# Performance work log

Hardware: AMD Instinct MI355X
Metric: run time of the kernel (lower is better)

The kernel has to match this reference:

```python
import jax, jax.numpy as jnp
import numpy as np

B, LD = 256, 64
NO, LO = 10240, 32
NM, LM = 81920, 16
EO, EM = 81920, 327680
E, HID, H, Dh, V = 128, 256, 8, 16, 10000


def masked_mean(tokens, table):
    # tokens: [N, L] int; pad id = 0
    emb = table[tokens]                            # [N, L, E]
    mask = (tokens != 0)
    s = jnp.sum(emb * mask[..., None].astype(emb.dtype), axis=1)
    lens = jnp.maximum(jnp.sum(mask, axis=1), 1).astype(emb.dtype)
    return s / lens[:, None]


def segment_softmax(scores, seg, num_segments):
    # scores: [E, ...]; softmax over entries sharing seg id (PyG softmax)
    m = jax.ops.segment_max(scores, seg, num_segments=num_segments)
    e = jnp.exp(scores - m[seg])
    s = jax.ops.segment_sum(e, seg, num_segments=num_segments)
    return e / (s[seg] + 1e-16)


def gcn_conv(x, W, b, src, dst, n):
    # PyG GCNConv: normalize=True, add_self_loops=True
    xw = x @ W
    loops = jnp.arange(n, dtype=src.dtype)
    s2 = jnp.concatenate([src, loops])
    d2 = jnp.concatenate([dst, loops])
    deg = jax.ops.segment_sum(jnp.ones_like(d2, dtype=x.dtype), d2, num_segments=n)
    dinv = deg ** -0.5  # deg >= 1 due to self loops
    norm = dinv[s2] * dinv[d2]
    out = jax.ops.segment_sum(xw[s2] * norm[:, None], d2, num_segments=n)
    return out + b


def transformer_conv(x, Wq, bq, Wk, bk, Wv, bv, Wskip, bskip, src, dst, n):
    q = (x @ Wq + bq).reshape(n, H, Dh)
    k = (x @ Wk + bk).reshape(n, H, Dh)
    v = (x @ Wv + bv).reshape(n, H, Dh)
    score = jnp.sum(q[dst] * k[src], axis=-1) / jnp.sqrt(jnp.asarray(Dh, x.dtype))  # [E, H]
    alpha = segment_softmax(score, dst, n)
    agg = jax.ops.segment_sum(alpha[:, :, None] * v[src], dst, num_segments=n)  # [n, H, Dh]
    return agg.reshape(n, H * Dh) + x @ Wskip + bskip


def global_attention(x, Wg, bg, seg, num_segments):
    gate = x @ Wg + bg                              # [N, 1]
    a = segment_softmax(gate, seg, num_segments)
    return jax.ops.segment_sum(a * x, seg, num_segments=num_segments)


def setup_inputs():
    key = jax.random.key(0)
    ks = jax.random.split(key, 20)
    sc = lambda k, shape: jax.random.normal(k, shape, dtype=jnp.float32) * 0.05
    inp = {
        "desc_tokens": jax.random.randint(ks[0], (B, LD), 0, V, dtype=jnp.int32),
        "x_tokens": jax.random.randint(ks[1], (NO, LO), 0, V, dtype=jnp.int32),
        "mini_tokens": jax.random.randint(ks[2], (NM, LM), 0, V, dtype=jnp.int32),
        "src": jax.random.randint(ks[3], (EO,), 0, NO, dtype=jnp.int32),
        "dst": jax.random.randint(ks[4], (EO,), 0, NO, dtype=jnp.int32),
        "mini_src": jax.random.randint(ks[5], (EM,), 0, NM, dtype=jnp.int32),
        "mini_dst": jax.random.randint(ks[6], (EM,), 0, NM, dtype=jnp.int32),
        "mini_batch": (jnp.arange(NM, dtype=jnp.int32) // (NM // NO)),
        "node_batch": (jnp.arange(NO, dtype=jnp.int32) // (NO // B)),
        "desc_table": sc(ks[7], (V, E)),
        "code_table": sc(ks[8], (V, E)),
        "code_table2": sc(ks[9], (V, E)),
        "Wq": sc(ks[10], (E, H * Dh)), "bq": jnp.zeros((H * Dh,), jnp.float32),
        "Wk": sc(ks[11], (E, H * Dh)), "bk": jnp.zeros((H * Dh,), jnp.float32),
        "Wv": sc(ks[12], (E, H * Dh)), "bv": jnp.zeros((H * Dh,), jnp.float32),
        "Wskip": sc(ks[13], (E, H * Dh)), "bskip": jnp.zeros((H * Dh,), jnp.float32),
        "W2": sc(ks[14], (E, HID)), "b2": jnp.zeros((HID,), jnp.float32),
        "W3": sc(ks[15], (HID, E)), "b3": jnp.zeros((E,), jnp.float32),
        "Wg": sc(ks[16], (E, 1)), "bg": jnp.zeros((1,), jnp.float32),
    }
    return inp


def reference(desc_tokens, x_tokens, mini_tokens, src, dst, mini_src, mini_dst,
              mini_batch, node_batch, desc_table, code_table, code_table2,
              Wq, bq, Wk, bk, Wv, bv, Wskip, bskip, W2, b2, W3, b3, Wg, bg):
    # encode_desc: embedding + masked mean pool -> [B, E]
    h_n = masked_mean(desc_tokens, desc_table)
    # encode_code_graph
    stmt_emb = masked_mean(x_tokens, code_table2)          # [NO, E]
    mini_emb = masked_mean(mini_tokens, code_table)        # [NM, E]
    mini_hidden = transformer_conv(mini_emb, Wq, bq, Wk, bk, Wv, bv,
                                   Wskip, bskip, mini_src, mini_dst, NM)
    mini_fn = global_attention(mini_hidden, Wg, bg, mini_batch, NO)  # [NO, E]
    mini_fn = (mini_fn + stmt_emb) * 0.5
    h = jax.nn.relu(gcn_conv(mini_fn, W2, b2, src, dst, NO))
    final_stmt = gcn_conv(h, W3, b3, src, dst, NO)
    fn_repr = global_attention(final_stmt, Wg, bg, node_batch, B)    # [B, E]
    # cosine similarity (torch eps=1e-8 clamps each norm)
    na = jnp.maximum(jnp.linalg.norm(fn_repr, axis=-1), 1e-8)
    nb = jnp.maximum(jnp.linalg.norm(h_n, axis=-1), 1e-8)
    return jnp.sum(fn_repr * h_n, axis=-1) / (na * nb)
```

## Files before the change

kernel.cpp:

```cpp
#include <hip/hip_runtime.h>
#include <hip/hip_bf16.h>
#include <math.h>

#define BB   256
#define LDE  64
#define NO   10240
#define LO   32
#define NM   81920
#define LM   16
#define EO   81920
#define EM   327680
#define ED   128
#define HIDD 256
#define NH   8
#define DH   16
#define VV   10000

static inline int nblk(long long n, int b) { return (int)((n + b - 1) / b); }

typedef __attribute__((ext_vector_type(8))) short short8;
typedef __attribute__((ext_vector_type(4))) float f32x4;

static __device__ __forceinline__ unsigned short bf16_rne(float f) {
  unsigned u = __float_as_uint(f);
  return (unsigned short)((u + 0x7fffu + ((u >> 16) & 1u)) >> 16);
}
static __device__ __forceinline__ float bf16_to_f(unsigned short h) {
  return __uint_as_float(((unsigned)h) << 16);
}
static __device__ __forceinline__ float4 b4f(ushort4 h) {
  return make_float4(bf16_to_f(h.x), bf16_to_f(h.y), bf16_to_f(h.z), bf16_to_f(h.w));
}
static __device__ __forceinline__ ushort4 f4b(float4 v) {
  return make_ushort4(bf16_rne(v.x), bf16_rne(v.y), bf16_rne(v.z), bf16_rne(v.w));
}

static __device__ __forceinline__ void gl_lds16(const void* g, void* l) {
  __builtin_amdgcn_global_load_lds(
      (const __attribute__((address_space(1))) unsigned int*)g,
      (__attribute__((address_space(3))) unsigned int*)l, 16, 0, 0);
}

struct ConvArgs {
  const float *Wq, *Wk, *Wv, *Ws, *W2, *W3;
  const float *bq, *bk, *bv, *bs;
  short8* frag;
  float* bias512;
  const float* t1; unsigned short* o1;
  const float* t2; unsigned short* o2;
  int* hist;
};
#define TBLK (2 * VV * ED / 4 / 256)
#define ZBLK ((NM + NO) / 256)
__global__ void __launch_bounds__(256)
conv_all_k(ConvArgs A) {
  int b = blockIdx.x;
  if (b < 32) {
    int g = b * 256 + threadIdx.x;
    int lane = g & 63, f = g >> 6;
    int jl = f & 7, kb = (f >> 3) & 3, ch = f >> 5;
    int cf = ch * 8 + jl;
    int c = cf * 16 + (lane & 15);
    int k0 = kb * 32 + ((lane >> 4) << 3);
    const float* wp; int cm;
    if (c < 128)      { wp = A.Wq; cm = c; }
    else if (c < 384) { int u = c - 128, t = u & 7;
                        wp = (t < 4) ? A.Wk : A.Wv; cm = (u >> 3) * 4 + (t & 3); }
    else              { wp = A.Ws; cm = c - 384; }
    short8 h;
    #pragma unroll
    for (int j = 0; j < 8; ++j)
      h[j] = (short)bf16_rne(wp[(size_t)(k0 + j) * 128 + cm]);
    A.frag[g] = h;
  } else if (b < 64) {
    int g = (b - 32) * 256 + threadIdx.x;
    const float* wp; int M, dstbase, gg;
    if (g < 4096) { wp = A.W2; M = 256; dstbase = 8192;  gg = g; }
    else          { wp = A.W3; M = 128; dstbase = 12288; gg = g - 4096; }
    int lane = gg & 63, fid = gg >> 6;
    int nt = fid % (M / 16), kb = fid / (M / 16);
    int n = nt * 16 + (lane & 15);
    int k0 = kb * 32 + ((lane >> 4) << 3);
    short8 h;
    #pragma unroll
    for (int j = 0; j < 8; ++j)
      h[j] = (short)bf16_rne(wp[(size_t)(k0 + j) * M + n]);
    A.frag[dstbase + gg] = h;
  } else if (b < 64 + TBLK) {
    int q = (b - 64) * 256 + threadIdx.x;
    const int NT = VV * ED / 4;
    if (q < NT) {
      float4 v = *(const float4*)(A.t1 + (size_t)q * 4);
      *(ushort4*)(A.o1 + (size_t)q * 4) = f4b(v);
    } else if (q < 2 * NT) {
      int q2 = q - NT;
      float4 v = *(const float4*)(A.t2 + (size_t)q2 * 4);
      *(ushort4*)(A.o2 + (size_t)q2 * 4) = f4b(v);
    }
  } else if (b < 64 + TBLK + ZBLK) {
    int i = (b - 64 - TBLK) * 256 + threadIdx.x;
    if (i < NM + NO) A.hist[i] = 0;
  } else {
    for (int c = threadIdx.x; c < 512; c += 256) {
      float v;
      if (c < 128)      v = A.bq[c];
      else if (c < 384) { int u = c - 128, t = u & 7;
                          v = (t < 4) ? A.bk[(u >> 3) * 4 + t] : A.bv[(u >> 3) * 4 + (t & 3)]; }
      else              v = A.bs[c - 384];
      A.bias512[c] = v;
    }
  }
}

template<int L>
static __device__ __forceinline__ void embed_body_f(const int* __restrict__ tokens,
                                                    const float* __restrict__ table,
                                                    float* __restrict__ out, int blk) {
  const int r = threadIdx.x >> 5, lane = threadIdx.x & 31;
  const int n0 = blk * 8;
  __shared__ int toks[8][L];
  for (int i = threadIdx.x; i < 8 * L; i += 256)
    toks[i / L][i % L] = tokens[(size_t)n0 * L + i];
  __syncthreads();
  float4 acc = make_float4(0.f, 0.f, 0.f, 0.f);
  int cnt = 0;
  #pragma unroll
  for (int l = 0; l < L; ++l) {
    int t = toks[r][l];
    float4 v = *(const float4*)(table + (size_t)t * ED + lane * 4);
    float msk = (t != 0) ? 1.f : 0.f;
    cnt += (t != 0);
    acc.x = fmaf(msk, v.x, acc.x); acc.y = fmaf(msk, v.y, acc.y);
    acc.z = fmaf(msk, v.z, acc.z); acc.w = fmaf(msk, v.w, acc.w);
  }
  float inv = 1.f / (float)(cnt > 0 ? cnt : 1);
  acc.x *= inv; acc.y *= inv; acc.z *= inv; acc.w *= inv;
  *(float4*)(out + (size_t)(n0 + r) * ED + lane * 4) = acc;
}

template<int L>
static __device__ __forceinline__ void embed_body16(const int* __restrict__ tokens,
                                                    const unsigned short* __restrict__ table,
                                                    unsigned short* __restrict__ out, int blk) {
  const int r = threadIdx.x >> 4, lane = threadIdx.x & 15;
  const int n0 = blk * 16;
  __shared__ int toks[16][L];
  for (int i = threadIdx.x; i < 16 * L; i += 256)
    toks[i / L][i % L] = tokens[(size_t)n0 * L + i];
  __syncthreads();
  float acc[8] = {};
  int cnt = 0;
  #pragma unroll
  for (int l = 0; l < L; ++l) {
    int t = toks[r][l];
    short8 v = *(const short8*)(table + (size_t)t * ED + lane * 8);
    float msk = (t != 0) ? 1.f : 0.f;
    cnt += (t != 0);
    #pragma unroll
    for (int j = 0; j < 8; ++j)
      acc[j] = fmaf(msk, bf16_to_f((unsigned short)v[j]), acc[j]);
  }
  float inv = 1.f / (float)(cnt > 0 ? cnt : 1);
  short8 o;
  #pragma unroll
  for (int j = 0; j < 8; ++j) o[j] = (short)bf16_rne(acc[j] * inv);
  *(short8*)(out + (size_t)(n0 + r) * ED + lane * 8) = o;
}

#define HBLK ((EM + EO) / 256)
#define MBLK (NM / 16)
#define XBLK (NO / 16)
__global__ void __launch_bounds__(256)
embed_all_k(const int* __restrict__ desc_tokens, const float* __restrict__ desc_table,
            float* __restrict__ h_n,
            const int* __restrict__ x_tokens, const unsigned short* __restrict__ ctab2,
            unsigned short* __restrict__ stmt,
            const int* __restrict__ mini_tokens, const unsigned short* __restrict__ ctab,
            unsigned short* __restrict__ miniE,
            const int* __restrict__ mini_dst, const int* __restrict__ dst,
            int* __restrict__ histm, int* __restrict__ histo) {
  int b = blockIdx.x;
  if (b < MBLK) embed_body16<LM>(mini_tokens, ctab, miniE, b);
  else if (b < MBLK + XBLK) embed_body16<LO>(x_tokens, ctab2, stmt, b - MBLK);
  else if (b < MBLK + XBLK + BB / 8)
    embed_body_f<LDE>(desc_tokens, desc_table, h_n, b - MBLK - XBLK);
  else {
    int e = (b - MBLK - XBLK - BB / 8) * 256 + threadIdx.x;
    if (e < EM) atomicAdd(&histm[mini_dst[e]], 1);
    else        atomicAdd(&histo[dst[e - EM]], 1);
  }
}

__global__ void __launch_bounds__(256)
scan_final2_k(const int* __restrict__ hist, const int* __restrict__ part,
              int* __restrict__ offsm, int* __restrict__ curm,
              int* __restrict__ offso, int* __restrict__ curo,
              float* __restrict__ dinv) {
  __shared__ int sd[256], red[256];
  const int b = blockIdx.x, t = threadIdx.x;
  const int i = b * 256 + t;
  const int v = hist[i];
  sd[t] = v; __syncthreads();
  for (int off = 1; off < 256; off <<= 1) {
    int a = (t >= off) ? sd[t - off] : 0;
    __syncthreads(); sd[t] += a; __syncthreads();
  }
  const int excl = sd[t] - v;
  const int segBase = (b < NM / 256) ? 0 : NM / 256;
  const int myIdx = b - segBase;
  int s = 0;
  for (int k = t; k < myIdx; k += 256) s += part[segBase + k];
  red[t] = s; __syncthreads();
  for (int o = 128; o > 0; o >>= 1) { if (t < o) red[t] += red[t + o]; __syncthreads(); }
  const int off = red[0] + excl;
  if (i < NM) {
    offsm[i] = off; curm[i] = off;
    if (i == NM - 1) offsm[NM] = off + v;
  } else {
    int i2 = i - NM;
    offso[i2] = off; curo[i2] = off;
    if (i2 == NO - 1) offso[NO] = off + v;
    dinv[i2] = 1.f / sqrtf(1.f + (float)v);
  }
}
__global__ void scatter2_k(const int* __restrict__ sm, const int* __restrict__ dm,
                           int* __restrict__ cm, int* __restrict__ km,
                           const int* __restrict__ so, const int* __restrict__ dd,
                           int* __restrict__ co, int* __restrict__ ko) {
  int e = blockIdx.x * 256 + threadIdx.x;
  if (e < EM) {
    int pos = atomicAdd(&cm[dm[e]], 1);
    km[pos] = sm[e];
  } else {
    int e2 = e - EM;
    if (e2 < EO) {
      int pos = atomicAdd(&co[dd[e2]], 1);
      ko[pos] = so[e2];
    }
  }
}

#define QKVSB (NM / 128)
#define CSUMB ((NM + NO) / 256)
__global__ void __launch_bounds__(512)
qkvs_merged_k(const unsigned short* __restrict__ Ab, const short8* __restrict__ Wf,
              const float* __restrict__ bias512, unsigned short* __restrict__ out,
              const int* __restrict__ hist, int* __restrict__ part) {
  __shared__ short8 wlds[2048];
  const int tid = threadIdx.x;
  if (blockIdx.x >= QKVSB) {
    int* sd = (int*)wlds;
    const int cb = blockIdx.x - QKVSB;
    const int i = cb * 256 + (tid & 255);
    if (tid < 256) sd[tid] = (i < NM + NO) ? hist[i] : 0;
    __syncthreads();
    for (int s = 128; s > 0; s >>= 1) {
      if (tid < s) sd[tid] += sd[tid + s];
      __syncthreads();
    }
    if (tid == 0) part[cb] = sd[0];
    return;
  }
  const int id = blockIdx.x;
  const int blk = (id & 7) * 80 + (id >> 3);
  const int n0 = blk * 128;
  const int w = tid >> 6, lane = tid & 63;
  const int r = lane & 15, qd = lane >> 4;
  const int node = n0 + w * 16 + r;
  char* myl = (char*)wlds + w * 4096;

  short8 a[4];
  #pragma unroll
  for (int kb = 0; kb < 4; ++kb)
    a[kb] = *(const short8*)(Ab + (size_t)node * ED + kb * 32 + qd * 8);

  for (int ch = 0; ch < 4; ++ch) {
    {
      const char* gs = (const char*)Wf + (size_t)ch * 32768
                     + (size_t)(w * 4) * 1024 + (size_t)lane * 16;
      char* ls = (char*)wlds + (w * 4) * 1024;
      #pragma unroll
      for (int t = 0; t < 4; ++t)
        gl_lds16(gs + t * 1024, ls + t * 1024);
    }
    __syncthreads();

    f32x4 acc[8];
    #pragma unroll
    for (int jl = 0; jl < 8; ++jl) acc[jl] = (f32x4){0.f, 0.f, 0.f, 0.f};
    #pragma unroll
    for (int kb = 0; kb < 4; ++kb)
      #pragma unroll
      for (int jl = 0; jl < 8; ++jl) {
        short8 wf = *(const short8*)((const char*)wlds
                      + ((size_t)((kb << 3) | jl) * 64 + lane) * 16);
        acc[jl] = __builtin_amdgcn_mfma_f32_16x16x32_bf16(wf, a[kb], acc[jl], 0, 0, 0);
      }
    __syncthreads();

    #pragma unroll
    for (int jl = 0; jl < 8; ++jl) {
      const int cf = ch * 8 + jl;
      const float4 bv = *(const float4*)(bias512 + cf * 16 + qd * 4);
      ushort4 o;
      o.x = bf16_rne(acc[jl][0] + bv.x);
      o.y = bf16_rne(acc[jl][1] + bv.y);
      o.z = bf16_rne(acc[jl][2] + bv.z);
      o.w = bf16_rne(acc[jl][3] + bv.w);
      *(ushort4*)(myl + r * 256 + ((jl * 32) ^ ((r & 7) << 5)) + qd * 8) = o;
    }
    #pragma unroll
    for (int t = 0; t < 4; ++t) {
      const int rr = t * 4 + qd;
      short8 v = *(const short8*)(myl + rr * 256 + (((lane & 15) * 16) ^ ((rr & 7) << 5)));
      *(short8*)(out + (size_t)(n0 + w * 16 + rr) * 512 + ch * 128 + (lane & 15) * 8) = v;
    }
    __syncthreads();
  }
}

template<bool RELU>
__global__ void __launch_bounds__(512)
mgemm_b_k(const unsigned short* __restrict__ Ab, const short8* __restrict__ Bh,
          const float* __restrict__ bias, unsigned short* __restrict__ C,
          int K, int M) {
  const int bn0 = blockIdx.x * 128;
  const int n0 = blockIdx.y * 128;
  const int tid = threadIdx.x;
  const int w = tid >> 6, lane = tid & 63;
  const int wm = (w & 3) * 2, wn = (w >> 2) * 4;
  const int r = lane & 15, qd = lane >> 4;
  const int NTm = M / 16;
  f32x4 acc[2][4];
  #pragma unroll
  for (int i = 0; i < 2; ++i)
    #pragma unroll
    for (int j = 0; j < 4; ++j) acc[i][j] = (f32x4){0.f, 0.f, 0.f, 0.f};
  const int kbn = K / 32;
  for (int kb = 0; kb < kbn; ++kb) {
    short8 bh[4];
    #pragma unroll
    for (int j = 0; j < 4; ++j)
      bh[j] = Bh[((size_t)kb * NTm + (bn0 >> 4) + wn + j) * 64 + lane];
    short8 a[2];
    #pragma unroll
    for (int i = 0; i < 2; ++i)
      a[i] = *(const short8*)(Ab + (size_t)(n0 + (wm + i) * 16 + r) * K + kb * 32 + qd * 8);
    #pragma unroll
    for (int i = 0; i < 2; ++i)
      #pragma unroll
      for (int j = 0; j < 4; ++j)
        acc[i][j] = __builtin_amdgcn_mfma_f32_16x16x32_bf16(bh[j], a[i], acc[i][j], 0, 0, 0);
  }
  #pragma unroll
  for (int i = 0; i < 2; ++i)
    #pragma unroll
    for (int j = 0; j < 4; ++j) {
      const int node = n0 + (wm + i) * 16 + r;
      const int colb = bn0 + (wn + j) * 16 + qd * 4;
      float4 bv = bias ? *(const float4*)(bias + colb) : make_float4(0.f, 0.f, 0.f, 0.f);
      float v0 = acc[i][j][0] + bv.x;
      float v1 = acc[i][j][1] + bv.y;
      float v2 = acc[i][j][2] + bv.z;
      float v3 = acc[i][j][3] + bv.w;
      if (RELU) {
        v0 = fmaxf(v0, 0.f); v1 = fmaxf(v1, 0.f);
        v2 = fmaxf(v2, 0.f); v3 = fmaxf(v3, 0.f);
      }
      ushort4 o = make_ushort4(bf16_rne(v0), bf16_rne(v1), bf16_rne(v2), bf16_rne(v3));
      *(ushort4*)(C + (size_t)node * M + colb) = o;
    }
}

__global__ void __launch_bounds__(256)
attn_comb_k(const unsigned short* __restrict__ buf,
            const int* __restrict__ offs, const int* __restrict__ csr,
            const float* __restrict__ Wg, const float* __restrict__ bg,
            const unsigned short* __restrict__ stmt, unsigned short* __restrict__ out) {
  const int g = threadIdx.x >> 5, lane = threadIdx.x & 31;
  const int n = blockIdx.x * 8 + g;
  float4 q = b4f(*(const ushort4*)(buf + (size_t)n * 512 + lane * 4));
  float4 sk = b4f(*(const ushort4*)(buf + (size_t)n * 512 + 384 + lane * 4));
  float4 wg = *(const float4*)(Wg + lane * 4);
  int lo = offs[n], hi = offs[n + 1];
  float4 O = make_float4(0.f, 0.f, 0.f, 0.f);
  float m = -INFINITY, l = 0.f;
  for (int base = lo; base < hi; base += 4) {
    int rem = hi - base;
    int sidx[4];
    #pragma unroll
    for (int i = 0; i < 4; ++i) sidx[i] = (i < rem) ? csr[base + i] : 0;
    short8 kvr[4];
    #pragma unroll
    for (int i = 0; i < 4; ++i)
      kvr[i] = *(const short8*)(buf + (size_t)sidx[i] * 512 + 128 + lane * 8);
    float sc[4]; float4 vt[4];
    #pragma unroll
    for (int i = 0; i < 4; ++i) {
      float4 kt = make_float4(bf16_to_f((unsigned short)kvr[i][0]),
                              bf16_to_f((unsigned short)kvr[i][1]),
                              bf16_to_f((unsigned short)kvr[i][2]),
                              bf16_to_f((unsigned short)kvr[i][3]));
      vt[i] = make_float4(bf16_to_f((unsigned short)kvr[i][4]),
                          bf16_to_f((unsigned short)kvr[i][5]),
                          bf16_to_f((unsigned short)kvr[i][6]),
                          bf16_to_f((unsigned short)kvr[i][7]));
      float p = q.x * kt.x + q.y * kt.y + q.z * kt.z + q.w * kt.w;
      p += __shfl_xor(p, 1, 64);
      p += __shfl_xor(p, 2, 64);
      sc[i] = (i < rem) ? p * 0.25f : -INFINITY;
    }
    float mt = fmaxf(fmaxf(sc[0], sc[1]), fmaxf(sc[2], sc[3]));
    float mn = fmaxf(m, mt);
    float scale = __expf(m - mn);
    float pe[4];
    #pragma unroll
    for (int i = 0; i < 4; ++i) pe[i] = __expf(sc[i] - mn);
    l = l * scale + ((pe[0] + pe[1]) + (pe[2] + pe[3]));
    O.x = fmaf(pe[3], vt[3].x, fmaf(pe[2], vt[2].x, fmaf(pe[1], vt[1].x, fmaf(pe[0], vt[0].x, O.x * scale))));
    O.y = fmaf(pe[3], vt[3].y, fmaf(pe[2], vt[2].y, fmaf(pe[1], vt[1].y, fmaf(pe[0], vt[0].y, O.y * scale))));
    O.z = fmaf(pe[3], vt[3].z, fmaf(pe[2], vt[2].z, fmaf(pe[1], vt[1].z, fmaf(pe[0], vt[0].z, O.z * scale))));
    O.w = fmaf(pe[3], vt[3].w, fmaf(pe[2], vt[2].w, fmaf(pe[1], vt[1].w, fmaf(pe[0], vt[0].w, O.w * scale))));
    m = mn;
  }
  float inv = 1.f / (l + 1e-16f);
  float4 ov = make_float4(O.x * inv + sk.x, O.y * inv + sk.y,
                          O.z * inv + sk.z, O.w * inv + sk.w);
  float ps = ov.x * wg.x + ov.y * wg.y + ov.z * wg.z + ov.w * wg.w;
  #pragma unroll
  for (int o = 1; o <= 16; o <<= 1) ps += __shfl_xor(ps, o, 64);
  __shared__ float outs[8][32][4];
  __shared__ float gates[8];
  *(float4*)&outs[g][lane][0] = ov;
  if (lane == 0) gates[g] = ps + bg[0];
  __syncthreads();
  if (threadIdx.x < 32) {
    float gm = -INFINITY;
    #pragma unroll
    for (int j = 0; j < 8; ++j) gm = fmaxf(gm, gates[j]);
    float e[8], s = 0.f;
    #pragma unroll
    for (int j = 0; j < 8; ++j) { e[j] = __expf(gates[j] - gm); s += e[j]; }
    float ia = 1.f / (s + 1e-16f);
    float4 acc = make_float4(0.f, 0.f, 0.f, 0.f);
    #pragma unroll
    for (int j = 0; j < 8; ++j) {
      float a = e[j] * ia;
      float4 v = *(const float4*)&outs[j][threadIdx.x][0];
      acc.x = fmaf(a, v.x, acc.x); acc.y = fmaf(a, v.y, acc.y);
      acc.z = fmaf(a, v.z, acc.z); acc.w = fmaf(a, v.w, acc.w);
    }
    float4 o4 = b4f(*(const ushort4*)(stmt + (size_t)blockIdx.x * ED + threadIdx.x * 4));
    acc.x = (acc.x + o4.x) * 0.5f; acc.y = (acc.y + o4.y) * 0.5f;
    acc.z = (acc.z + o4.z) * 0.5f; acc.w = (acc.w + o4.w) * 0.5f;
    *(ushort4*)(out + (size_t)blockIdx.x * ED + threadIdx.x * 4) = f4b(acc);
  }
}

__global__ void __launch_bounds__(256)
gcn_gather_b_k(const unsigned short* __restrict__ x, const float* __restrict__ dinv,
               const int* __restrict__ offs, const int* __restrict__ csr,
               const float* __restrict__ bias, unsigned short* __restrict__ out,
               const float* __restrict__ Wg, const float* __restrict__ bg,
               float* __restrict__ gateOut) {
  const int wv = threadIdx.x >> 6, lane = threadIdx.x & 63;
  const int half = lane >> 5, cl = lane & 31;
  const int n = blockIdx.x * 4 + wv;
  float di = dinv[n];
  float4 acc = make_float4(0.f, 0.f, 0.f, 0.f);
  if (half == 0) {
    float4 xs = b4f(*(const ushort4*)(x + (size_t)n * ED + cl * 4));
    float w0 = di * di;
    acc = make_float4(w0 * xs.x, w0 * xs.y, w0 * xs.z, w0 * xs.w);
  }
  int lo = offs[n], hi = offs[n + 1];
  for (int base = lo; base < hi; base += 8) {
    int sidx[4]; bool ok[4];
    #pragma unroll
    for (int i = 0; i < 4; ++i) {
      int e = base + 2 * i + half;
      ok[i] = e < hi;
      sidx[i] = ok[i] ? csr[e] : 0;
    }
    float dw[4];
    #pragma unroll
    for (int i = 0; i < 4; ++i) dw[i] = ok[i] ? di * dinv[sidx[i]] : 0.f;
    ushort4 vr[4];
    #pragma unroll
    for (int i = 0; i < 4; ++i)
      vr[i] = *(const ushort4*)(x + (size_t)sidx[i] * ED + cl * 4);
    #pragma unroll
    for (int i = 0; i < 4; ++i) {
      float4 v = b4f(vr[i]);
      acc.x = fmaf(dw[i], v.x, acc.x); acc.y = fmaf(dw[i], v.y, acc.y);
      acc.z = fmaf(dw[i], v.z, acc.z); acc.w = fmaf(dw[i], v.w, acc.w);
    }
  }
  acc.x += __shfl_xor(acc.x, 32, 64); acc.y += __shfl_xor(acc.y, 32, 64);
  acc.z += __shfl_xor(acc.z, 32, 64); acc.w += __shfl_xor(acc.w, 32, 64);
  if (bias) {
    float4 b4 = *(const float4*)(bias + cl * 4);
    acc.x += b4.x; acc.y += b4.y; acc.z += b4.z; acc.w += b4.w;
  }
  if (half == 0)
    *(ushort4*)(out + (size_t)n * ED + cl * 4) = f4b(acc);
  if (gateOut) {
    float4 wg = *(const float4*)(Wg + cl * 4);
    float ps = acc.x * wg.x + acc.y * wg.y + acc.z * wg.z + acc.w * wg.w;
    #pragma unroll
    for (int o = 1; o <= 16; o <<= 1) ps += __shfl_xor(ps, o, 64);
    if (lane == 0) gateOut[n] = ps + bg[0];
  }
}

static __device__ __forceinline__ int lower_bound_d(const int* a, int n, int key) {
  int lo = 0, hi = n;
  while (lo < hi) { int mid = (lo + hi) >> 1; if (a[mid] < key) lo = mid + 1; else hi = mid; }
  return lo;
}
__global__ void __launch_bounds__(128)
gattn_cos_k(const unsigned short* __restrict__ x, const float* __restrict__ gate,
            const int* __restrict__ seg, int Ntot,
            const float* __restrict__ hn, float* __restrict__ outp) {
  const int g = threadIdx.x >> 5, lane = threadIdx.x & 31;
  const int n = blockIdx.x * 4 + g;
  __shared__ int sh[4][2];
  if (lane == 0) {
    sh[g][0] = lower_bound_d(seg, Ntot, n);
    sh[g][1] = lower_bound_d(seg, Ntot, n + 1);
  }
  __syncthreads();
  int lo = sh[g][0], hi = sh[g][1];
  float m = -INFINITY;
  for (int j = lo; j < hi; ++j) m = fmaxf(m, gate[j]);
  float ssum = 0.f;
  for (int j = lo; j < hi; ++j) ssum += __expf(gate[j] - m);
  float inv = 1.f / (ssum + 1e-16f);
  float4 acc = make_float4(0.f, 0.f, 0.f, 0.f);
  for (int j = lo; j < hi; ++j) {
    float a = __expf(gate[j] - m) * inv;
    float4 v = b4f(*(const ushort4*)(x + (size_t)j * ED + lane * 4));
    acc.x = fmaf(a, v.x, acc.x); acc.y = fmaf(a, v.y, acc.y);
    acc.z = fmaf(a, v.z, acc.z); acc.w = fmaf(a, v.w, acc.w);
  }
  float4 hv = *(const float4*)(hn + (size_t)n * ED + lane * 4);
  float dot = acc.x * hv.x + acc.y * hv.y + acc.z * hv.z + acc.w * hv.w;
  float na  = acc.x * acc.x + acc.y * acc.y + acc.z * acc.z + acc.w * acc.w;
  float nb  = hv.x * hv.x + hv.y * hv.y + hv.z * hv.z + hv.w * hv.w;
  #pragma unroll
  for (int o = 1; o <= 16; o <<= 1) {
    dot += __shfl_xor(dot, o, 64);
    na  += __shfl_xor(na,  o, 64);
    nb  += __shfl_xor(nb,  o, 64);
  }
  if (lane == 0)
    outp[n] = dot / (fmaxf(sqrtf(na), 1e-8f) * fmaxf(sqrtf(nb), 1e-8f));
}

constexpr size_t OFF_HN    = 0;
constexpr size_t OFF_STMT  = OFF_HN    + (size_t)BB * ED;
constexpr size_t OFF_A     = OFF_STMT  + (size_t)NO * ED;
constexpr size_t OFF_CT    = OFF_A     + (size_t)NM * ED;
constexpr size_t OFF_QKVS  = OFF_CT    + (size_t)VV * ED;
constexpr size_t T0        = OFF_QKVS  + (size_t)NM * 256;
constexpr size_t OFF_GATE  = T0;
constexpr size_t OFF_GATE2 = OFF_GATE  + (size_t)NM;
constexpr size_t OFF_DINV  = OFF_GATE2 + (size_t)NO;
constexpr size_t OFF_HISTM = OFF_DINV  + (size_t)NO;
constexpr size_t OFF_HISTO = OFF_HISTM + (size_t)NM;
constexpr size_t OFF_OFFSM = OFF_HISTO + (size_t)NO;
constexpr size_t OFF_CURM  = OFF_OFFSM + (size_t)NM + 1;
constexpr size_t OFF_CSRM  = OFF_CURM  + (size_t)NM;
constexpr size_t OFF_OFFSO = OFF_CSRM  + (size_t)EM;
constexpr size_t OFF_CURO  = OFF_OFFSO + (size_t)NO + 1;
constexpr size_t OFF_CSRO  = OFF_CURO  + (size_t)NO;
constexpr size_t OFF_PART  = OFF_CSRO  + (size_t)EO;
constexpr size_t OFF_B512  = OFF_PART  + 512;
constexpr size_t OFF_WFHI  = OFF_B512  + 512;
constexpr size_t OFF_MFN   = OFF_A;
constexpr size_t OFF_AGG   = OFF_MFN   + (size_t)NO * ED;
constexpr size_t OFF_H     = OFF_AGG   + (size_t)NO * ED;
constexpr size_t OFF_T     = OFF_H     + (size_t)NO * HIDD;
constexpr size_t OFF_FIN   = OFF_T     + (size_t)NO * ED;

extern "C" void kernel_launch(void* const* d_in, const int* in_sizes, int n_in,
                              void* d_out, int out_size, void* d_ws, size_t ws_size,
                              hipStream_t stream) {
  const int* desc_tokens = (const int*)d_in[0];
  const int* x_tokens    = (const int*)d_in[1];
  const int* mini_tokens = (const int*)d_in[2];
  const int* src         = (const int*)d_in[3];
  const int* dst         = (const int*)d_in[4];
  const int* mini_src    = (const int*)d_in[5];
  const int* mini_dst    = (const int*)d_in[6];
  const int* mini_batch  = (const int*)d_in[7];
  const int* node_batch  = (const int*)d_in[8];
  const float* desc_table  = (const float*)d_in[9];
  const float* code_table  = (const float*)d_in[10];
  const float* code_table2 = (const float*)d_in[11];
  const float* Wq = (const float*)d_in[12]; const float* bq = (const float*)d_in[13];
  const float* Wk = (const float*)d_in[14]; const float* bk = (const float*)d_in[15];
  const float* Wv = (const float*)d_in[16]; const float* bv = (const float*)d_in[17];
  const float* Wskip = (const float*)d_in[18]; const float* bskip = (const float*)d_in[19];
  const float* W2 = (const float*)d_in[20]; const float* b2 = (const float*)d_in[21];
  const float* W3 = (const float*)d_in[22]; const float* b3 = (const float*)d_in[23];
  const float* Wg = (const float*)d_in[24]; const float* bg = (const float*)d_in[25];
  (void)mini_batch;

  float* ws = (float*)d_ws;
  float* h_n   = ws + OFF_HN;
  unsigned short* stmt_b  = (unsigned short*)(ws + OFF_STMT);
  unsigned short* miniE_b = (unsigned short*)(ws + OFF_A);
  unsigned short* ctab_b  = (unsigned short*)(ws + OFF_CT);
  unsigned short* ctab2_b = ctab_b + (size_t)VV * ED;
  unsigned short* qkvs_b  = (unsigned short*)(ws + OFF_QKVS);
  float* gate2 = ws + OFF_GATE2;
  float* dinv  = ws + OFF_DINV;
  int* histm = (int*)(ws + OFF_HISTM);
  int* histo = (int*)(ws + OFF_HISTO);
  int* offsm = (int*)(ws + OFF_OFFSM);
  int* curm  = (int*)(ws + OFF_CURM);
  int* csrm  = (int*)(ws + OFF_CSRM);
  int* offso = (int*)(ws + OFF_OFFSO);
  int* curo  = (int*)(ws + OFF_CURO);
  int* csro  = (int*)(ws + OFF_CSRO);
  int* part  = (int*)(ws + OFF_PART);
  float* bias512 = ws + OFF_B512;
  short8* wfrag = (short8*)(ws + OFF_WFHI);
  unsigned short* mini_fn_b = (unsigned short*)(ws + OFF_MFN);
  unsigned short* aggb_b    = (unsigned short*)(ws + OFF_AGG);
  unsigned short* hbuf_b    = (unsigned short*)(ws + OFF_H);
  unsigned short* tbuf_b    = (unsigned short*)(ws + OFF_T);
  unsigned short* finalS_b  = (unsigned short*)(ws + OFF_FIN);
  float* outp    = (float*)d_out;

  ConvArgs ca;
  ca.Wq = Wq; ca.Wk = Wk; ca.Wv = Wv; ca.Ws = Wskip; ca.W2 = W2; ca.W3 = W3;
  ca.bq = bq; ca.bk = bk; ca.bv = bv; ca.bs = bskip;
  ca.frag = wfrag; ca.bias512 = bias512;
  ca.t1 = code_table;  ca.o1 = ctab_b;
  ca.t2 = code_table2; ca.o2 = ctab2_b;
  ca.hist = histm;
  conv_all_k<<<64 + TBLK + ZBLK + 1, 256, 0, stream>>>(ca);

  embed_all_k<<<MBLK + XBLK + BB / 8 + HBLK, 256, 0, stream>>>(
      desc_tokens, desc_table, h_n, x_tokens, ctab2_b, stmt_b,
      mini_tokens, ctab_b, miniE_b, mini_dst, dst, histm, histo);

  qkvs_merged_k<<<QKVSB + CSUMB, 512, 0, stream>>>(miniE_b, wfrag, bias512, qkvs_b,
                                                   histm, part);

  scan_final2_k<<<(NM + NO) / 256, 256, 0, stream>>>(histm, part, offsm, curm,
                                                     offso, curo, dinv);
  scatter2_k<<<nblk(EM + EO, 256), 256, 0, stream>>>(mini_src, mini_dst, curm, csrm,
                                                     src, dst, curo, csro);

  attn_comb_k<<<NO, 256, 0, stream>>>(qkvs_b, offsm, csrm, Wg, bg, stmt_b, mini_fn_b);

  gcn_gather_b_k<<<NO / 4, 256, 0, stream>>>(mini_fn_b, dinv, offso, csro, nullptr,
                                             aggb_b, nullptr, nullptr, nullptr);
  { dim3 g(HIDD / 128, NO / 128);
    mgemm_b_k<true><<<g, 512, 0, stream>>>(aggb_b, wfrag + 8192, b2, hbuf_b, ED, HIDD); }

  { dim3 g(1, NO / 128);
    mgemm_b_k<false><<<g, 512, 0, stream>>>(hbuf_b, wfrag + 12288, nullptr, tbuf_b, HIDD, ED); }
  gcn_gather_b_k<<<NO / 4, 256, 0, stream>>>(tbuf_b, dinv, offso, csro, b3, finalS_b,
                                             Wg, bg, gate2);

  gattn_cos_k<<<BB / 4, 128, 0, stream>>>(finalS_b, gate2, node_batch, NO, h_n, outp);
}
```

Measured before the change: 311.8 us.

## Fuse first GCN gather with both dense layers into one kernel

Replaces the first GCN gather plus the two MFMA GEMM launches with one kernel. Each 512-thread block aggregates 128 nodes into LDS, runs the W2 GEMM with bias and ReLU into LDS, then runs the W3 GEMM and writes the result. This removes two launches and the global round trips for the aggregated and hidden buffers. In exchange the grid shrinks to only 80 blocks, which leaves most of the GPU idle during the latency-bound gather phase.

```diff
diff --git a/kernel.cpp b/kernel.cpp
--- a/kernel.cpp
+++ b/kernel.cpp
@@ -319,59 +319,6 @@
   }
 }
 
-template<bool RELU>
-__global__ void __launch_bounds__(512)
-mgemm_b_k(const unsigned short* __restrict__ Ab, const short8* __restrict__ Bh,
-          const float* __restrict__ bias, unsigned short* __restrict__ C,
-          int K, int M) {
-  const int bn0 = blockIdx.x * 128;
-  const int n0 = blockIdx.y * 128;
-  const int tid = threadIdx.x;
-  const int w = tid >> 6, lane = tid & 63;
-  const int wm = (w & 3) * 2, wn = (w >> 2) * 4;
-  const int r = lane & 15, qd = lane >> 4;
-  const int NTm = M / 16;
-  f32x4 acc[2][4];
-  #pragma unroll
-  for (int i = 0; i < 2; ++i)
-    #pragma unroll
-    for (int j = 0; j < 4; ++j) acc[i][j] = (f32x4){0.f, 0.f, 0.f, 0.f};
-  const int kbn = K / 32;
-  for (int kb = 0; kb < kbn; ++kb) {
-    short8 bh[4];
-    #pragma unroll
-    for (int j = 0; j < 4; ++j)
-      bh[j] = Bh[((size_t)kb * NTm + (bn0 >> 4) + wn + j) * 64 + lane];
-    short8 a[2];
-    #pragma unroll
-    for (int i = 0; i < 2; ++i)
-      a[i] = *(const short8*)(Ab + (size_t)(n0 + (wm + i) * 16 + r) * K + kb * 32 + qd * 8);
-    #pragma unroll
-    for (int i = 0; i < 2; ++i)
-      #pragma unroll
-      for (int j = 0; j < 4; ++j)
-        acc[i][j] = __builtin_amdgcn_mfma_f32_16x16x32_bf16(bh[j], a[i], acc[i][j], 0, 0, 0);
-  }
-  #pragma unroll
-  for (int i = 0; i < 2; ++i)
-    #pragma unroll
-    for (int j = 0; j < 4; ++j) {
-      const int node = n0 + (wm + i) * 16 + r;
-      const int colb = bn0 + (wn + j) * 16 + qd * 4;
-      float4 bv = bias ? *(const float4*)(bias + colb) : make_float4(0.f, 0.f, 0.f, 0.f);
-      float v0 = acc[i][j][0] + bv.x;
-      float v1 = acc[i][j][1] + bv.y;
-      float v2 = acc[i][j][2] + bv.z;
-      float v3 = acc[i][j][3] + bv.w;
-      if (RELU) {
-        v0 = fmaxf(v0, 0.f); v1 = fmaxf(v1, 0.f);
-        v2 = fmaxf(v2, 0.f); v3 = fmaxf(v3, 0.f);
-      }
-      ushort4 o = make_ushort4(bf16_rne(v0), bf16_rne(v1), bf16_rne(v2), bf16_rne(v3));
-      *(ushort4*)(C + (size_t)node * M + colb) = o;
-    }
-}
-
 __global__ void __launch_bounds__(256)
 attn_comb_k(const unsigned short* __restrict__ buf,
             const int* __restrict__ offs, const int* __restrict__ csr,
@@ -454,6 +401,101 @@
     acc.x = (acc.x + o4.x) * 0.5f; acc.y = (acc.y + o4.y) * 0.5f;
     acc.z = (acc.z + o4.z) * 0.5f; acc.w = (acc.w + o4.w) * 0.5f;
     *(ushort4*)(out + (size_t)blockIdx.x * ED + threadIdx.x * 4) = f4b(acc);
+  }
+}
+
+__global__ void __launch_bounds__(512)
+mlp_fused_k(const unsigned short* __restrict__ x,
+            const float* __restrict__ dinv,
+            const int* __restrict__ offs, const int* __restrict__ csr,
+            const short8* __restrict__ W2f, const float* __restrict__ b2,
+            const short8* __restrict__ W3f,
+            unsigned short* __restrict__ tout) {
+  __shared__ char buf[128 * 512];
+  const int tid = threadIdx.x;
+  const int w = tid >> 6, lane = tid & 63;
+  const int half = lane >> 5, cl = lane & 31;
+  const int n0 = blockIdx.x * 128;
+
+  for (int i = 0; i < 16; ++i) {
+    const int rl = w * 16 + i;
+    const int n = n0 + rl;
+    float di = dinv[n];
+    float4 acc = make_float4(0.f, 0.f, 0.f, 0.f);
+    if (half == 0) {
+      float4 xs = b4f(*(const ushort4*)(x + (size_t)n * ED + cl * 4));
+      float w0 = di * di;
+      acc = make_float4(w0 * xs.x, w0 * xs.y, w0 * xs.z, w0 * xs.w);
+    }
+    int lo = offs[n], hi = offs[n + 1];
+    for (int base = lo; base < hi; base += 8) {
+      int sidx[4]; bool ok[4];
+      #pragma unroll
+      for (int t = 0; t < 4; ++t) {
+        int e = base + 2 * t + half;
+        ok[t] = e < hi;
+        sidx[t] = ok[t] ? csr[e] : 0;
+      }
+      float dw[4];
+      #pragma unroll
+      for (int t = 0; t < 4; ++t) dw[t] = ok[t] ? di * dinv[sidx[t]] : 0.f;
+      ushort4 vr[4];
+      #pragma unroll
+      for (int t = 0; t < 4; ++t)
+        vr[t] = *(const ushort4*)(x + (size_t)sidx[t] * ED + cl * 4);
+      #pragma unroll
+      for (int t = 0; t < 4; ++t) {
+        float4 v = b4f(vr[t]);
+        acc.x = fmaf(dw[t], v.x, acc.x); acc.y = fmaf(dw[t], v.y, acc.y);
+        acc.z = fmaf(dw[t], v.z, acc.z); acc.w = fmaf(dw[t], v.w, acc.w);
+      }
+    }
+    acc.x += __shfl_xor(acc.x, 32, 64); acc.y += __shfl_xor(acc.y, 32, 64);
+    acc.z += __shfl_xor(acc.z, 32, 64); acc.w += __shfl_xor(acc.w, 32, 64);
+    if (half == 0)
+      *(ushort4*)(buf + rl * 256 + ((cl * 8) ^ ((rl & 7) << 4))) = f4b(acc);
+  }
+  __syncthreads();
+
+  const int r = lane & 15, qd = lane >> 4;
+  const int row = w * 16 + r;
+  short8 a1[4];
+  #pragma unroll
+  for (int kb = 0; kb < 4; ++kb)
+    a1[kb] = *(const short8*)(buf + row * 256 + ((kb * 64 + qd * 16) ^ ((row & 7) << 4)));
+  __syncthreads();
+
+  #pragma unroll 4
+  for (int cf = 0; cf < 16; ++cf) {
+    f32x4 acc = (f32x4){0.f, 0.f, 0.f, 0.f};
+    #pragma unroll
+    for (int kb = 0; kb < 4; ++kb)
+      acc = __builtin_amdgcn_mfma_f32_16x16x32_bf16(
+          W2f[((size_t)(kb * 16 + cf)) * 64 + lane], a1[kb], acc, 0, 0, 0);
+    const float4 bv = *(const float4*)(b2 + cf * 16 + qd * 4);
+    ushort4 o;
+    o.x = bf16_rne(fmaxf(acc[0] + bv.x, 0.f));
+    o.y = bf16_rne(fmaxf(acc[1] + bv.y, 0.f));
+    o.z = bf16_rne(fmaxf(acc[2] + bv.z, 0.f));
+    o.w = bf16_rne(fmaxf(acc[3] + bv.w, 0.f));
+    *(ushort4*)(buf + row * 512 + ((cf * 32 + qd * 8) ^ ((row & 7) << 4))) = o;
+  }
+  __syncthreads();
+
+  short8 a2[8];
+  #pragma unroll
+  for (int kb = 0; kb < 8; ++kb)
+    a2[kb] = *(const short8*)(buf + row * 512 + ((kb * 64 + qd * 16) ^ ((row & 7) << 4)));
+  #pragma unroll
+  for (int cf = 0; cf < 8; ++cf) {
+    f32x4 acc = (f32x4){0.f, 0.f, 0.f, 0.f};
+    #pragma unroll
+    for (int kb = 0; kb < 8; ++kb)
+      acc = __builtin_amdgcn_mfma_f32_16x16x32_bf16(
+          W3f[((size_t)(kb * 8 + cf)) * 64 + lane], a2[kb], acc, 0, 0, 0);
+    ushort4 o = make_ushort4(bf16_rne(acc[0]), bf16_rne(acc[1]),
+                             bf16_rne(acc[2]), bf16_rne(acc[3]));
+    *(ushort4*)(tout + (size_t)(n0 + row) * ED + cf * 16 + qd * 4) = o;
   }
 }
 
@@ -578,9 +620,7 @@
 constexpr size_t OFF_B512  = OFF_PART  + 512;
 constexpr size_t OFF_WFHI  = OFF_B512  + 512;
 constexpr size_t OFF_MFN   = OFF_A;
-constexpr size_t OFF_AGG   = OFF_MFN   + (size_t)NO * ED;
-constexpr size_t OFF_H     = OFF_AGG   + (size_t)NO * ED;
-constexpr size_t OFF_T     = OFF_H     + (size_t)NO * HIDD;
+constexpr size_t OFF_T     = OFF_MFN   + (size_t)NO * ED;
 constexpr size_t OFF_FIN   = OFF_T     + (size_t)NO * ED;
 
 extern "C" void kernel_launch(void* const* d_in, const int* in_sizes, int n_in,
@@ -628,8 +668,6 @@
   float* bias512 = ws + OFF_B512;
   short8* wfrag = (short8*)(ws + OFF_WFHI);
   unsigned short* mini_fn_b = (unsigned short*)(ws + OFF_MFN);
-  unsigned short* aggb_b    = (unsigned short*)(ws + OFF_AGG);
-  unsigned short* hbuf_b    = (unsigned short*)(ws + OFF_H);
   unsigned short* tbuf_b    = (unsigned short*)(ws + OFF_T);
   unsigned short* finalS_b  = (unsigned short*)(ws + OFF_FIN);
   float* outp    = (float*)d_out;
@@ -657,13 +695,9 @@
 
   attn_comb_k<<<NO, 256, 0, stream>>>(qkvs_b, offsm, csrm, Wg, bg, stmt_b, mini_fn_b);
 
-  gcn_gather_b_k<<<NO / 4, 256, 0, stream>>>(mini_fn_b, dinv, offso, csro, nullptr,
-                                             aggb_b, nullptr, nullptr, nullptr);
-  { dim3 g(HIDD / 128, NO / 128);
-    mgemm_b_k<true><<<g, 512, 0, stream>>>(aggb_b, wfrag + 8192, b2, hbuf_b, ED, HIDD); }
-
-  { dim3 g(1, NO / 128);
-    mgemm_b_k<false><<<g, 512, 0, stream>>>(hbuf_b, wfrag + 12288, nullptr, tbuf_b, HIDD, ED); }
+  mlp_fused_k<<<NO / 128, 512, 0, stream>>>(mini_fn_b, dinv, offso, csro,
+                                            wfrag + 8192, b2, wfrag + 12288, tbuf_b);
+
   gcn_gather_b_k<<<NO / 4, 256, 0, stream>>>(tbuf_b, dinv, offso, csro, b3, finalS_b,
                                              Wg, bg, gate2);
 
```

Result: slower. 352.0 us (+12.9%).
